# Performance work log

Hardware: AMD Instinct MI355X
Metric: run time of the kernel (lower is better)

Reference implementation:

```python
import jax, jax.numpy as jnp
import numpy as np
from jax import lax

NEG_INF = -1e30

def _binarize(w):
    # BinaryConnect / XNOR-style sign binarization with straight-through estimator
    return w + lax.stop_gradient(jnp.sign(w) - w)

def _conv(x, w, b):
    y = lax.conv_general_dilated(x, w, window_strides=(1, 1), padding='VALID',
                                 dimension_numbers=('NCHW', 'OIHW', 'NCHW'))
    return y + b[None, :, None, None]

def _bn(x, eps, gamma=None, beta=None):
    # training-mode batch norm over (N, H, W)
    mean = jnp.mean(x, axis=(0, 2, 3), keepdims=True)
    var = jnp.var(x, axis=(0, 2, 3), keepdims=True)
    xn = (x - mean) * lax.rsqrt(var + eps)
    if gamma is not None:
        g = jnp.clip(gamma, 0.01, None)  # torch forward clamps BN weight to >=0.01
        xn = xn * g[None, :, None, None] + beta[None, :, None, None]
    return xn

def _maxpool2(x):
    return lax.reduce_window(x, NEG_INF, lax.max, (1, 1, 2, 2), (1, 1, 2, 2), 'VALID')


def setup_inputs() -> dict:
    key = jax.random.key(0)
    ks = jax.random.split(key, 12)
    f = jnp.float32
    return {
        'x': jax.random.normal(ks[0], (8192, 1, 32, 32), dtype=f),
        'conv1_w': jax.random.normal(ks[1], (6, 1, 5, 5), dtype=f) * 0.2,
        'conv1_b': jnp.zeros((6,), dtype=f),
        'conv2_w': jax.random.normal(ks[2], (16, 6, 5, 5), dtype=f) * 0.1,
        'conv2_b': jnp.zeros((16,), dtype=f),
        'bn2_g': jnp.ones((16,), dtype=f),
        'bn2_b': jnp.zeros((16,), dtype=f),
        'conv3_w': jax.random.normal(ks[3], (120, 16, 5, 5), dtype=f) * 0.05,
        'conv3_b': jnp.zeros((120,), dtype=f),
        'bn3_g': jnp.ones((120,), dtype=f),
        'bn3_b': jnp.zeros((120,), dtype=f),
        'fc1_w': jax.random.normal(ks[4], (84, 120), dtype=f) * 0.09,
        'fc1_b': jnp.zeros((84,), dtype=f),
        'fc2_w': jax.random.normal(ks[5], (10, 84), dtype=f) * 0.1,
        'fc2_b': jnp.zeros((10,), dtype=f),
    }


def reference(x, conv1_w, conv1_b, conv2_w, conv2_b, bn2_g, bn2_b,
              conv3_w, conv3_b, bn3_g, bn3_b, fc1_w, fc1_b, fc2_w, fc2_b):
    # layer1: fp conv -> BN(no affine, eps=1e-4) -> relu -> maxpool  [B,6,14,14]
    h = _maxpool2(jax.nn.relu(_bn(_conv(x, conv1_w, conv1_b), 1e-4)))
    # layer2: binary conv -> BN(affine, eps=1e-4) -> relu -> maxpool [B,16,5,5]
    h = _maxpool2(jax.nn.relu(_bn(_conv(h, _binarize(conv2_w), conv2_b), 1e-4, bn2_g, bn2_b)))
    # layer3: binary conv -> BN(affine, eps=1e-5) -> relu            [B,120,1,1]
    h = jax.nn.relu(_bn(_conv(h, _binarize(conv3_w), conv3_b), 1e-5, bn3_g, bn3_b))
    # layer4: binary linear -> relu -> linear                        [B,10]
    h = h.reshape(h.shape[0], -1)  # [B,120]
    h = jax.nn.relu(h @ _binarize(fc1_w).T + fc1_b)
    return h @ fc2_w.T + fc2_b
```

## Files before the change

kernel.cpp:

```cpp
#include <hip/hip_runtime.h>

#define DEVFN __device__ __forceinline__

DEVFN float sgnf(float x) { return (x > 0.f) ? 1.f : ((x < 0.f) ? -1.f : 0.f); }

DEVFN unsigned short f2bf(float x) {
  unsigned int u = __float_as_uint(x);
  unsigned int r = (u + 0x7fffu + ((u >> 16) & 1u)) >> 16;
  return (unsigned short)r;
}

typedef __attribute__((ext_vector_type(8))) short short8;
typedef __attribute__((ext_vector_type(4))) float f32x4;

#define SUM1 0
#define SQ1  384
#define SUM2 768
#define SQ2  1792
#define SUM3 2816
#define SQ3  10496
#define DBL_BYTES 145408

#define A1 0
#define C1 8
#define A2 16
#define C2 32
#define A3 48
#define C3 168
#define W2B_OFF  512
#define WFR_OFF  3584
#define WFR2_OFF 54784
#define H1_OFF   69632
#define H2_OFF   (H1_OFF + 8192*1176)
#define Y3_OFF   (H2_OFF + 8192*400)

__global__ __launch_bounds__(256, 3) void conv1_prep(
    const float* __restrict__ x, const float* __restrict__ w1,
    const float* __restrict__ b1, float* __restrict__ m1,
    double* __restrict__ sums, const float* __restrict__ w2,
    const float* __restrict__ w3, const float* __restrict__ f1,
    float* __restrict__ w2t, unsigned short* __restrict__ wfr,
    unsigned short* __restrict__ wfr2) {
  __shared__ float simg[8 * 1088];
  __shared__ float swtp[6 * 40];
  __shared__ float red[6], redq[6];
  int tid = threadIdx.x;
  if (blockIdx.x >= 1024) {
    int i = (blockIdx.x - 1024) * 256 + tid;
    if (i < 2688) {
      int ci = i / 448, r = i - ci * 448;
      int ch = r / 28, k = r - ch * 28;
      w2t[i] = (k < 25) ? sgnf(w2[(ch * 6 + ci) * 25 + k]) : 0.f;
    }
    if (i < 102400) {
      int j = i & 7;
      int t = i >> 3;
      int l = t & 63;
      int cc = (t >> 6) % 25;
      int nt = (t >> 6) / 25;
      int ch = nt * 16 + (l & 15);
      int kp = cc * 32 + ((l >> 4) << 3) + j;
      float v = (ch < 120) ? sgnf(w3[ch * 400 + (kp >> 1)]) : 0.f;
      wfr[i] = f2bf(v);
    }
    if (i < 24576) {
      int j = i & 7;
      int t = i >> 3;
      int l = t & 63;
      int cc = (t >> 6) & 7;
      int nt = t >> 9;
      int col = nt * 16 + (l & 15);
      int kp = cc * 32 + ((l >> 4) << 3) + j;
      int k = kp >> 1;
      float v = (col < 84 && k < 120) ? sgnf(f1[col * 120 + k]) : 0.f;
      wfr2[i] = f2bf(v);
    }
    return;
  }
  int img0 = blockIdx.x * 8;
  {
    const float2* xg = (const float2*)(x + (size_t)img0 * 1024);
    for (int i2 = tid; i2 < 4096; i2 += 256) {
      int img = i2 >> 9;
      int r = (i2 >> 4) & 31;
      int c2 = i2 & 15;
      *(float2*)&simg[img * 1088 + r * 34 + c2 * 2] = xg[i2];
    }
  }
  for (int i = tid; i < 240; i += 256) {
    int ch = i / 40, k = i - ch * 40;
    swtp[i] = (k < 25) ? w1[ch * 25 + k] : 0.f;
  }
  if (tid < 6) { red[tid] = 0.f; redq[tid] = 0.f; }
  __syncthreads();

  for (int idx = tid; idx < 672; idx += 256) {
    int img = idx / 84;
    int r = idx - img * 84;
    int ch = r / 14;
    int py = r - ch * 14;
    float wr[25];
    {
      const float4* wp = (const float4*)&swtp[ch * 40];
#pragma unroll
      for (int t = 0; t < 6; ++t) {
        float4 v = wp[t];
        wr[4 * t] = v.x; wr[4 * t + 1] = v.y; wr[4 * t + 2] = v.z; wr[4 * t + 3] = v.w;
      }
      wr[24] = swtp[ch * 40 + 24];
    }
    float bb = b1[ch];
    float acc0[28], acc1[28];
#pragma unroll
    for (int o = 0; o < 28; ++o) { acc0[o] = bb; acc1[o] = bb; }
#pragma unroll
    for (int d = 0; d < 6; ++d) {
      int row = 2 * py + d;
      float rb[32];
      const float2* rp = (const float2*)&simg[img * 1088 + row * 34];
#pragma unroll
      for (int t = 0; t < 16; ++t) { float2 v = rp[t]; rb[2 * t] = v.x; rb[2 * t + 1] = v.y; }
      if (d < 5) {
#pragma unroll
        for (int kx = 0; kx < 5; ++kx) {
          float w = wr[d * 5 + kx];
#pragma unroll
          for (int o = 0; o < 28; ++o) acc0[o] = fmaf(rb[o + kx], w, acc0[o]);
        }
      }
      if (d >= 1) {
#pragma unroll
        for (int kx = 0; kx < 5; ++kx) {
          float w = wr[(d - 1) * 5 + kx];
#pragma unroll
          for (int o = 0; o < 28; ++o) acc1[o] = fmaf(rb[o + kx], w, acc1[o]);
        }
      }
    }
    float s = 0.f, s2 = 0.f;
#pragma unroll
    for (int o = 0; o < 28; ++o) {
      s += acc0[o] + acc1[o];
      s2 = fmaf(acc0[o], acc0[o], s2);
      s2 = fmaf(acc1[o], acc1[o], s2);
    }
    atomicAdd(&red[ch], s);
    atomicAdd(&redq[ch], s2);
    float* mp = m1 + (size_t)(img0 + img) * 1176 + ch * 196 + py * 14;
#pragma unroll
    for (int j = 0; j < 7; ++j) {
      float2 v;
      v.x = fmaxf(fmaxf(acc0[4 * j], acc0[4 * j + 1]), fmaxf(acc1[4 * j], acc1[4 * j + 1]));
      v.y = fmaxf(fmaxf(acc0[4 * j + 2], acc0[4 * j + 3]), fmaxf(acc1[4 * j + 2], acc1[4 * j + 3]));
      *(float2*)&mp[2 * j] = v;
    }
  }
  __syncthreads();
  if (tid < 6) {
    int slot = blockIdx.x & 63;
    atomicAdd(&sums[SUM1 + tid * 64 + slot], (double)red[tid]);
    atomicAdd(&sums[SQ1 + tid * 64 + slot], (double)redq[tid]);
  }
}

__global__ __launch_bounds__(256) void finalize_bn(
    const double* __restrict__ sum, const double* __restrict__ sq, int nch,
    double invN, double eps, const float* __restrict__ gamma,
    const float* __restrict__ beta, float* __restrict__ a,
    float* __restrict__ c) {
  int t = blockIdx.x * 256 + threadIdx.x;
  int ch = t >> 6, slot = t & 63;
  if (ch >= nch) return;
  double s = sum[ch * 64 + slot];
  double q = sq[ch * 64 + slot];
#pragma unroll
  for (int off = 32; off > 0; off >>= 1) {
    s += __shfl_down(s, off, 64);
    q += __shfl_down(q, off, 64);
  }
  if (slot == 0) {
    double mean = s * invN;
    double var = q * invN - mean * mean;
    float inv = (float)(1.0 / sqrt(var + eps));
    float g = gamma ? fmaxf(gamma[ch], 0.01f) : 1.f;
    float av = g * inv;
    float cv = (beta ? beta[ch] : 0.f) - (float)mean * av;
    a[ch] = av;
    c[ch] = cv;
  }
}

__global__ __launch_bounds__(320, 6) void conv2_fused(
    const float* __restrict__ m1, const float* __restrict__ w2t,
    const float* __restrict__ b2, const float* __restrict__ scales,
    float* __restrict__ m2, double* __restrict__ sums) {
  __shared__ float sh1[4 * 1352];
  __shared__ float sa1[6], sc1[6];
  __shared__ float red[16], redq[16];
  int tid = threadIdx.x;
  int img0 = blockIdx.x * 4;
  if (tid < 6) { sa1[tid] = scales[A1 + tid]; sc1[tid] = scales[C1 + tid]; }
  if (tid < 16) { red[tid] = 0.f; redq[tid] = 0.f; }
  __syncthreads();
  {
    const float2* mg = (const float2*)(m1 + (size_t)img0 * 1176);
    for (int i2 = tid; i2 < 2352; i2 += 320) {
      int img = i2 / 588;
      int r = i2 - img * 588;
      int pl = r / 98;
      int rr = r - pl * 98;
      int row = rr / 7, t = rr - row * 7;
      float a = sa1[pl], c = sc1[pl];
      float2 v = mg[i2];
      v.x = fmaxf(fmaf(a, v.x, c), 0.f);
      v.y = fmaxf(fmaf(a, v.y, c), 0.f);
      *(float2*)&sh1[img * 1352 + pl * 224 + row * 16 + t * 2] = v;
    }
  }
  __syncthreads();

  int ch = tid & 15;
  int img = (tid >> 4) & 3;
  int pr = tid >> 6;
  float bb = b2[ch];
  float acc[2][10];
#pragma unroll
  for (int o = 0; o < 10; ++o) { acc[0][o] = bb; acc[1][o] = bb; }
  const float* ibase = &sh1[img * 1352];
  const float* wbase = w2t + ch * 28;
  for (int ci = 0; ci < 6; ++ci) {
    float w[25];
    {
      const float4* wp = (const float4*)(wbase + ci * 448);
#pragma unroll
      for (int t = 0; t < 6; ++t) {
        float4 v = wp[t];
        w[4 * t] = v.x; w[4 * t + 1] = v.y; w[4 * t + 2] = v.z; w[4 * t + 3] = v.w;
      }
      w[24] = wbase[ci * 448 + 24];
    }
    const float* rbase = ibase + ci * 224 + pr * 32;
#pragma unroll
    for (int d = 0; d < 6; ++d) {
      float rb[16];
      const float4* rp = (const float4*)(rbase + d * 16);
#pragma unroll
      for (int t = 0; t < 4; ++t) {
        float4 v = rp[t];
        rb[4 * t] = v.x; rb[4 * t + 1] = v.y; rb[4 * t + 2] = v.z; rb[4 * t + 3] = v.w;
      }
      if (d < 5) {
#pragma unroll
        for (int kx = 0; kx < 5; ++kx) {
          float wv = w[d * 5 + kx];
#pragma unroll
          for (int o = 0; o < 10; ++o) acc[0][o] = fmaf(rb[o + kx], wv, acc[0][o]);
        }
      }
      if (d >= 1) {
#pragma unroll
        for (int kx = 0; kx < 5; ++kx) {
          float wv = w[(d - 1) * 5 + kx];
#pragma unroll
          for (int o = 0; o < 10; ++o) acc[1][o] = fmaf(rb[o + kx], wv, acc[1][o]);
        }
      }
    }
  }
  float s0 = 0.f, q0 = 0.f;
#pragma unroll
  for (int rr2 = 0; rr2 < 2; ++rr2)
#pragma unroll
    for (int o = 0; o < 10; ++o) {
      float v = acc[rr2][o];
      s0 += v;
      q0 = fmaf(v, v, q0);
    }
  {
    float* mpo = m2 + (size_t)(img0 + img) * 400 + ch * 25 + pr * 5;
#pragma unroll
    for (int pc = 0; pc < 5; ++pc)
      mpo[pc] = fmaxf(fmaxf(acc[0][2 * pc], acc[0][2 * pc + 1]),
                      fmaxf(acc[1][2 * pc], acc[1][2 * pc + 1]));
  }
  s0 += __shfl_xor(s0, 16, 64); q0 += __shfl_xor(q0, 16, 64);
  s0 += __shfl_xor(s0, 32, 64); q0 += __shfl_xor(q0, 32, 64);
  if ((tid & 48) == 0) {
    atomicAdd(&red[ch], s0);
    atomicAdd(&redq[ch], q0);
  }
  __syncthreads();
  if (tid < 16) {
    int slot = blockIdx.x & 63;
    atomicAdd(&sums[SUM2 + tid * 64 + slot], (double)red[tid]);
    atomicAdd(&sums[SQ2 + tid * 64 + slot], (double)redq[tid]);
  }
}

__global__ __launch_bounds__(256) void conv3_mfma(
    const float* __restrict__ m2, const unsigned short* __restrict__ wfr,
    const float* __restrict__ b3, const float* __restrict__ scales,
    float* __restrict__ y3, double* __restrict__ sums) {
  __shared__ unsigned int Alds[16 * 404];
  __shared__ float sa2[16], sc2[16];
  __shared__ float red[128], redq[128];
  int tid = threadIdx.x;
  int img0 = blockIdx.x * 16;
  if (tid < 16) { sa2[tid] = scales[A2 + tid]; sc2[tid] = scales[C2 + tid]; }
  if (tid < 128) { red[tid] = 0.f; redq[tid] = 0.f; }
  __syncthreads();
  for (int i4 = tid; i4 < 1600; i4 += 256) {
    int img = i4 / 100, k4 = i4 - img * 100;
    int k = 4 * k4;
    float4 v = *(const float4*)(m2 + (size_t)(img0 + img) * 400 + k);
    float vv[4] = {v.x, v.y, v.z, v.w};
    unsigned int pk[4];
#pragma unroll
    for (int e = 0; e < 4; ++e) {
      int ch = ((k + e) * 41) >> 10;
      float val = fmaxf(fmaf(sa2[ch], vv[e], sc2[ch]), 0.f);
      unsigned int hb = f2bf(val);
      float vh = __uint_as_float(hb << 16);
      unsigned int lb = f2bf(val - vh);
      pk[e] = hb | (lb << 16);
    }
    unsigned int* dst = &Alds[img * 404 + k];
    dst[0] = pk[0]; dst[1] = pk[1]; dst[2] = pk[2]; dst[3] = pk[3];
  }
  __syncthreads();

  int lane = tid & 63;
  int wv = tid >> 6;
  int nt0 = wv * 2, nt1 = wv * 2 + 1;
  const short8* bvec = (const short8*)wfr;
  int arow = lane & 15;
  int ag = lane >> 4;
  f32x4 acc0 = {0.f, 0.f, 0.f, 0.f}, acc1 = {0.f, 0.f, 0.f, 0.f};
  const unsigned short* abase =
      (const unsigned short*)&Alds[arow * 404 + ag * 4];
#pragma unroll 5
  for (int c = 0; c < 25; ++c) {
    short8 af = *(const short8*)(abase + c * 32);
    short8 b0 = bvec[(nt0 * 25 + c) * 64 + lane];
    short8 b1 = bvec[(nt1 * 25 + c) * 64 + lane];
    acc0 = __builtin_amdgcn_mfma_f32_16x16x32_bf16(af, b0, acc0, 0, 0, 0);
    acc1 = __builtin_amdgcn_mfma_f32_16x16x32_bf16(af, b1, acc1, 0, 0, 0);
  }
  int chA = nt0 * 16 + (lane & 15);
  int chB = nt1 * 16 + (lane & 15);
  int rbase = img0 + ((lane >> 4) << 2);
  {
    float bias = b3[chA];
    float s = 0.f, q = 0.f;
#pragma unroll
    for (int r = 0; r < 4; ++r) {
      float v = acc0[r] + bias;
      y3[(size_t)(rbase + r) * 120 + chA] = v;
      s += v; q = fmaf(v, v, q);
    }
    atomicAdd(&red[chA], s);
    atomicAdd(&redq[chA], q);
  }
  if (chB < 120) {
    float bias = b3[chB];
    float s = 0.f, q = 0.f;
#pragma unroll
    for (int r = 0; r < 4; ++r) {
      float v = acc1[r] + bias;
      y3[(size_t)(rbase + r) * 120 + chB] = v;
      s += v; q = fmaf(v, v, q);
    }
    atomicAdd(&red[chB], s);
    atomicAdd(&redq[chB], q);
  }
  __syncthreads();
  if (tid < 120) {
    int slot = blockIdx.x & 63;
    atomicAdd(&sums[SUM3 + tid * 64 + slot], (double)red[tid]);
    atomicAdd(&sums[SQ3 + tid * 64 + slot], (double)redq[tid]);
  }
}

__global__ __launch_bounds__(192) void fc_mfma(
    const float* __restrict__ y3, const float* __restrict__ scales,
    const unsigned short* __restrict__ wfr2, const float* __restrict__ b1,
    const float* __restrict__ w2, const float* __restrict__ b2,
    float* __restrict__ out) {
  __shared__ unsigned int Alds[16 * 132];
  __shared__ float sh4[16 * 88];
  __shared__ float sw2[10 * 85];
  __shared__ float sa3[120], sc3[120];
  __shared__ float sb1[84], sb2[10];
  int tid = threadIdx.x;
  int img0 = blockIdx.x * 16;
  if (tid < 120) { sa3[tid] = scales[A3 + tid]; sc3[tid] = scales[C3 + tid]; }
  if (tid < 84) sb1[tid] = b1[tid];
  if (tid >= 84 && tid < 94) sb2[tid - 84] = b2[tid - 84];
  for (int i = tid; i < 850; i += 192) {
    int o = i / 85, k = i - o * 85;
    sw2[i] = (k < 84) ? w2[o * 84 + k] : 0.f;
  }
  __syncthreads();
  for (int i4 = tid; i4 < 512; i4 += 192) {
    int img = i4 >> 5, k4 = i4 & 31;
    int k = 4 * k4;
    unsigned int pk[4] = {0u, 0u, 0u, 0u};
    if (k4 < 30) {
      float4 v = *(const float4*)(y3 + (size_t)(img0 + img) * 120 + k);
      float vv[4] = {v.x, v.y, v.z, v.w};
#pragma unroll
      for (int e = 0; e < 4; ++e) {
        float val = fmaxf(fmaf(sa3[k + e], vv[e], sc3[k + e]), 0.f);
        unsigned int hb = f2bf(val);
        float vh = __uint_as_float(hb << 16);
        unsigned int lb = f2bf(val - vh);
        pk[e] = hb | (lb << 16);
      }
    }
    unsigned int* dst = &Alds[img * 132 + k];
    dst[0] = pk[0]; dst[1] = pk[1]; dst[2] = pk[2]; dst[3] = pk[3];
  }
  __syncthreads();

  int lane = tid & 63;
  int wv = tid >> 6;
  int nt0 = wv * 2, nt1 = wv * 2 + 1;
  const short8* bvec = (const short8*)wfr2;
  int arow = lane & 15;
  int ag = lane >> 4;
  f32x4 acc0 = {0.f, 0.f, 0.f, 0.f}, acc1 = {0.f, 0.f, 0.f, 0.f};
  const unsigned short* abase =
      (const unsigned short*)&Alds[arow * 132 + ag * 4];
#pragma unroll
  for (int c = 0; c < 8; ++c) {
    short8 af = *(const short8*)(abase + c * 32);
    short8 b0 = bvec[(nt0 * 8 + c) * 64 + lane];
    short8 b1 = bvec[(nt1 * 8 + c) * 64 + lane];
    acc0 = __builtin_amdgcn_mfma_f32_16x16x32_bf16(af, b0, acc0, 0, 0, 0);
    acc1 = __builtin_amdgcn_mfma_f32_16x16x32_bf16(af, b1, acc1, 0, 0, 0);
  }
  {
    int jA = nt0 * 16 + (lane & 15);
    int jB = nt1 * 16 + (lane & 15);
    int r0 = (lane >> 4) << 2;
#pragma unroll
    for (int r = 0; r < 4; ++r)
      sh4[(r0 + r) * 88 + jA] = fmaxf(acc0[r] + sb1[jA], 0.f);
    if (jB < 84) {
#pragma unroll
      for (int r = 0; r < 4; ++r)
        sh4[(r0 + r) * 88 + jB] = fmaxf(acc1[r] + sb1[jB], 0.f);
    }
  }
  __syncthreads();
  if (tid < 160) {
    int img = tid / 10, o = tid - (tid / 10) * 10;
    float acc = sb2[o];
    const float* hp = &sh4[img * 88];
    const float* wp = &sw2[o * 85];
#pragma unroll 4
    for (int k = 0; k < 84; ++k) acc = fmaf(hp[k], wp[k], acc);
    out[(size_t)(img0 + img) * 10 + o] = acc;
  }
}

extern "C" void kernel_launch(void* const* d_in, const int* in_sizes, int n_in,
                              void* d_out, int out_size, void* d_ws,
                              size_t ws_size, hipStream_t stream) {
  const float* x = (const float*)d_in[0];
  const float* conv1_w = (const float*)d_in[1];
  const float* conv1_b = (const float*)d_in[2];
  const float* conv2_w = (const float*)d_in[3];
  const float* conv2_b = (const float*)d_in[4];
  const float* bn2_g = (const float*)d_in[5];
  const float* bn2_b = (const float*)d_in[6];
  const float* conv3_w = (const float*)d_in[7];
  const float* conv3_b = (const float*)d_in[8];
  const float* bn3_g = (const float*)d_in[9];
  const float* bn3_b = (const float*)d_in[10];
  const float* fc1_w = (const float*)d_in[11];
  const float* fc1_b = (const float*)d_in[12];
  const float* fc2_w = (const float*)d_in[13];
  const float* fc2_b = (const float*)d_in[14];
  float* out = (float*)d_out;

  double* sums = (double*)d_ws;
  float* fbase = (float*)((char*)d_ws + DBL_BYTES);
  float* scales = fbase;
  float* w2t = fbase + W2B_OFF;
  unsigned short* wfr = (unsigned short*)(fbase + WFR_OFF);
  unsigned short* wfr2 = (unsigned short*)(fbase + WFR2_OFF);
  float* m1 = fbase + H1_OFF;
  float* m2 = fbase + H2_OFF;
  float* y3 = fbase + Y3_OFF;

  hipMemsetAsync(d_ws, 0, DBL_BYTES, stream);

  conv1_prep<<<1424, 256, 0, stream>>>(x, conv1_w, conv1_b, m1, sums, conv2_w,
                                       conv3_w, fc1_w, w2t, wfr, wfr2);
  finalize_bn<<<2, 256, 0, stream>>>(sums + SUM1, sums + SQ1, 6,
                                     1.0 / (8192.0 * 784.0), 1e-4, nullptr,
                                     nullptr, scales + A1, scales + C1);

  conv2_fused<<<2048, 320, 0, stream>>>(m1, w2t, conv2_b, scales, m2, sums);
  finalize_bn<<<4, 256, 0, stream>>>(sums + SUM2, sums + SQ2, 16,
                                     1.0 / (8192.0 * 100.0), 1e-4, bn2_g, bn2_b,
                                     scales + A2, scales + C2);

  conv3_mfma<<<512, 256, 0, stream>>>(m2, wfr, conv3_b, scales, y3, sums);
  finalize_bn<<<30, 256, 0, stream>>>(sums + SUM3, sums + SQ3, 120,
                                      1.0 / 8192.0, 1e-5, bn3_g, bn3_b,
                                      scales + A3, scales + C3);

  fc_mfma<<<512, 192, 0, stream>>>(y3, scales, wfr2, fc1_b, fc2_w, fc2_b, out);
}
```

Measured before the change: 226.5 us.

## Pack image pairs into float2 lanes in conv2 for packed FMA

conv2 now handles 8 images per block by interleaving pairs of images into float2 elements in shared memory. Each thread computes two images at once with packed two-wide FMAs, which can map to packed FP32 instructions, and reuses each weight load and index calculation across both images. The change doubles LDS per block, halves the grid and lowers the occupancy hint from 6 to 4. The global load into shared memory is now scalar and strided across images rather than a float2 contiguous read, which may cost some load efficiency.

Measured after the change: 231.5 us. 2.2% more time.

```diff
diff --git a/kernel.cpp b/kernel.cpp
--- a/kernel.cpp
+++ b/kernel.cpp
@@ -12,6 +12,7 @@
 
 typedef __attribute__((ext_vector_type(8))) short short8;
 typedef __attribute__((ext_vector_type(4))) float f32x4;
+typedef __attribute__((ext_vector_type(2))) float f32x2;
 
 #define SUM1 0
 #define SQ1  384
@@ -190,43 +191,48 @@
   }
 }
 
-__global__ __launch_bounds__(320, 6) void conv2_fused(
+__global__ __launch_bounds__(320, 4) void conv2_fused(
     const float* __restrict__ m1, const float* __restrict__ w2t,
     const float* __restrict__ b2, const float* __restrict__ scales,
     float* __restrict__ m2, double* __restrict__ sums) {
-  __shared__ float sh1[4 * 1352];
+  __shared__ f32x2 sh1[4 * 1352];
   __shared__ float sa1[6], sc1[6];
   __shared__ float red[16], redq[16];
   int tid = threadIdx.x;
-  int img0 = blockIdx.x * 4;
+  int img0 = blockIdx.x * 8;
   if (tid < 6) { sa1[tid] = scales[A1 + tid]; sc1[tid] = scales[C1 + tid]; }
   if (tid < 16) { red[tid] = 0.f; redq[tid] = 0.f; }
   __syncthreads();
   {
-    const float2* mg = (const float2*)(m1 + (size_t)img0 * 1176);
-    for (int i2 = tid; i2 < 2352; i2 += 320) {
-      int img = i2 / 588;
-      int r = i2 - img * 588;
-      int pl = r / 98;
-      int rr = r - pl * 98;
-      int row = rr / 7, t = rr - row * 7;
+    for (int i2 = tid; i2 < 4704; i2 += 320) {
+      int p = i2 / 1176;
+      int e = i2 - p * 1176;
+      int pl = e / 196;
+      int rr = e - pl * 196;
+      int row = rr / 14, col = rr - row * 14;
+      const float* s0 = m1 + (size_t)(img0 + 2 * p) * 1176 + e;
+      f32x2 v;
+      v.x = s0[0];
+      v.y = s0[1176];
       float a = sa1[pl], c = sc1[pl];
-      float2 v = mg[i2];
-      v.x = fmaxf(fmaf(a, v.x, c), 0.f);
-      v.y = fmaxf(fmaf(a, v.y, c), 0.f);
-      *(float2*)&sh1[img * 1352 + pl * 224 + row * 16 + t * 2] = v;
+      f32x2 av = {a, a}, cv = {c, c}, zz = {0.f, 0.f};
+      v = __builtin_elementwise_max(__builtin_elementwise_fma(av, v, cv), zz);
+      sh1[p * 1352 + pl * 224 + row * 16 + col] = v;
     }
   }
   __syncthreads();
 
   int ch = tid & 15;
-  int img = (tid >> 4) & 3;
+  int p = (tid >> 4) & 3;
   int pr = tid >> 6;
   float bb = b2[ch];
-  float acc[2][10];
-#pragma unroll
-  for (int o = 0; o < 10; ++o) { acc[0][o] = bb; acc[1][o] = bb; }
-  const float* ibase = &sh1[img * 1352];
+  f32x2 acc[2][10];
+#pragma unroll
+  for (int o = 0; o < 10; ++o) {
+    acc[0][o] = (f32x2){bb, bb};
+    acc[1][o] = (f32x2){bb, bb};
+  }
+  const float* ibase = (const float*)&sh1[p * 1352 + pr * 32];
   const float* wbase = w2t + ch * 28;
   for (int ci = 0; ci < 6; ++ci) {
     float w[25];
@@ -239,30 +245,35 @@
       }
       w[24] = wbase[ci * 448 + 24];
     }
-    const float* rbase = ibase + ci * 224 + pr * 32;
+    const float* rbase = ibase + ci * 448;
 #pragma unroll
     for (int d = 0; d < 6; ++d) {
-      float rb[16];
-      const float4* rp = (const float4*)(rbase + d * 16);
-#pragma unroll
-      for (int t = 0; t < 4; ++t) {
-        float4 v = rp[t];
-        rb[4 * t] = v.x; rb[4 * t + 1] = v.y; rb[4 * t + 2] = v.z; rb[4 * t + 3] = v.w;
+      f32x2 rb[16];
+      const f32x4* rp = (const f32x4*)(rbase + d * 32);
+#pragma unroll
+      for (int t = 0; t < 8; ++t) {
+        f32x4 v = rp[t];
+        rb[2 * t] = (f32x2){v.x, v.y};
+        rb[2 * t + 1] = (f32x2){v.z, v.w};
       }
       if (d < 5) {
 #pragma unroll
         for (int kx = 0; kx < 5; ++kx) {
           float wv = w[d * 5 + kx];
-#pragma unroll
-          for (int o = 0; o < 10; ++o) acc[0][o] = fmaf(rb[o + kx], wv, acc[0][o]);
+          f32x2 ws = {wv, wv};
+#pragma unroll
+          for (int o = 0; o < 10; ++o)
+            acc[0][o] = __builtin_elementwise_fma(rb[o + kx], ws, acc[0][o]);
         }
       }
       if (d >= 1) {
 #pragma unroll
         for (int kx = 0; kx < 5; ++kx) {
           float wv = w[(d - 1) * 5 + kx];
-#pragma unroll
-          for (int o = 0; o < 10; ++o) acc[1][o] = fmaf(rb[o + kx], wv, acc[1][o]);
+          f32x2 ws = {wv, wv};
+#pragma unroll
+          for (int o = 0; o < 10; ++o)
+            acc[1][o] = __builtin_elementwise_fma(rb[o + kx], ws, acc[1][o]);
         }
       }
     }
@@ -272,16 +283,22 @@
   for (int rr2 = 0; rr2 < 2; ++rr2)
 #pragma unroll
     for (int o = 0; o < 10; ++o) {
-      float v = acc[rr2][o];
-      s0 += v;
-      q0 = fmaf(v, v, q0);
+      f32x2 v = acc[rr2][o];
+      s0 += v.x + v.y;
+      q0 = fmaf(v.x, v.x, q0);
+      q0 = fmaf(v.y, v.y, q0);
     }
   {
-    float* mpo = m2 + (size_t)(img0 + img) * 400 + ch * 25 + pr * 5;
-#pragma unroll
-    for (int pc = 0; pc < 5; ++pc)
-      mpo[pc] = fmaxf(fmaxf(acc[0][2 * pc], acc[0][2 * pc + 1]),
-                      fmaxf(acc[1][2 * pc], acc[1][2 * pc + 1]));
+    float* mpoA = m2 + (size_t)(img0 + 2 * p) * 400 + ch * 25 + pr * 5;
+    float* mpoB = mpoA + 400;
+#pragma unroll
+    for (int pc = 0; pc < 5; ++pc) {
+      f32x2 m = __builtin_elementwise_max(
+          __builtin_elementwise_max(acc[0][2 * pc], acc[0][2 * pc + 1]),
+          __builtin_elementwise_max(acc[1][2 * pc], acc[1][2 * pc + 1]));
+      mpoA[pc] = m.x;
+      mpoB[pc] = m.y;
+    }
   }
   s0 += __shfl_xor(s0, 16, 64); q0 += __shfl_xor(q0, 16, 64);
   s0 += __shfl_xor(s0, 32, 64); q0 += __shfl_xor(q0, 32, 64);
@@ -502,7 +519,7 @@
                                      1.0 / (8192.0 * 784.0), 1e-4, nullptr,
                                      nullptr, scales + A1, scales + C1);
 
-  conv2_fused<<<2048, 320, 0, stream>>>(m1, w2t, conv2_b, scales, m2, sums);
+  conv2_fused<<<1024, 320, 0, stream>>>(m1, w2t, conv2_b, scales, m2, sums);
   finalize_bn<<<4, 256, 0, stream>>>(sums + SUM2, sums + SQ2, 16,
                                      1.0 / (8192.0 * 100.0), 1e-4, bn2_g, bn2_b,
                                      scales + A2, scales + C2);
```
